# Kernel optimization log

Hardware: AMD Instinct MI355X
Metric: run time of the kernel (lower is better)

The kernel has to match this reference:

```python
import jax, jax.numpy as jnp
import numpy as np

EPS = 1e-5

def layer_norm(x, gamma, beta):
    m = jnp.mean(x, axis=-1, keepdims=True)
    v = jnp.var(x, axis=-1, keepdims=True)
    return (x - m) * jax.lax.rsqrt(v + EPS) * gamma + beta


def setup_inputs() -> dict:
    key = jax.random.key(0)
    ks = jax.random.split(key, 8)
    B, N, E, C = 1, 512, 128, 128
    s = 0.02
    inp = {
        "pair_rep": jax.random.normal(ks[0], (B, N, N, E), dtype=jnp.float32),
        "ln_pair_g": jnp.ones((E,), jnp.float32),
        "ln_pair_b": jnp.zeros((E,), jnp.float32),
        "ga_w": jax.random.normal(ks[1], (E, C), jnp.float32) * s,
        "ga_b": jnp.zeros((C,), jnp.float32),
        "la_w": jax.random.normal(ks[2], (E, C), jnp.float32) * s,
        "la_b": jnp.zeros((C,), jnp.float32),
        "gb_w": jax.random.normal(ks[3], (E, C), jnp.float32) * s,
        "gb_b": jnp.zeros((C,), jnp.float32),
        "lb_w": jax.random.normal(ks[4], (E, C), jnp.float32) * s,
        "lb_b": jnp.zeros((C,), jnp.float32),
        "g_w": jax.random.normal(ks[5], (E, E), jnp.float32) * s,
        "g_b": jnp.zeros((E,), jnp.float32),
        "ln_up_g": jnp.ones((C,), jnp.float32),
        "ln_up_b": jnp.zeros((C,), jnp.float32),
        "lu_w": jax.random.normal(ks[6], (C, E), jnp.float32) * s,
        "lu_b": jnp.zeros((E,), jnp.float32),
    }
    return inp


def reference(pair_rep, ln_pair_g, ln_pair_b, ga_w, ga_b, la_w, la_b,
              gb_w, gb_b, lb_w, lb_b, g_w, g_b, ln_up_g, ln_up_b, lu_w, lu_b):
    # pair_rep: [B, N, N, E]
    z = layer_norm(pair_rep, ln_pair_g, ln_pair_b)
    a = jax.nn.sigmoid(z @ ga_w + ga_b) * (z @ la_w + la_b)  # [B,N,N,C]
    b = jax.nn.sigmoid(z @ gb_w + gb_b) * (z @ lb_w + lb_b)  # [B,N,N,C]
    g = jax.nn.sigmoid(z @ g_w + g_b)                        # [B,N,N,E]
    # torch: sum(a.unsqueeze(-3)*b.unsqueeze(-4), dim=-2) == sum_k a[i,k,c]*b[j,k,c]
    update = jnp.einsum("bikc,bjkc->bijc", a, b)             # [B,N,N,C]
    out = g * (layer_norm(update, ln_up_g, ln_up_b) @ lu_w + lu_b)
    return out
```

## Files before the change

kernel.cpp:

```cpp
#include <hip/hip_runtime.h>
#include <hip/hip_bf16.h>

#define NN 512
#define MM (NN*NN)

typedef __attribute__((ext_vector_type(8))) unsigned short u16x8;
typedef __attribute__((ext_vector_type(4))) unsigned short u16x4;
typedef __attribute__((ext_vector_type(8))) __bf16 bf16x8;
typedef __attribute__((ext_vector_type(4))) float f32x4;

static __device__ __forceinline__ unsigned short f2bfi(float f) {
  return __builtin_bit_cast(unsigned short, __float2bfloat16(f));
}
static __device__ __forceinline__ float bf2f(unsigned short h) {
  return __uint_as_float(((unsigned int)h) << 16);
}
static __device__ __forceinline__ bf16x8 ldfrag(const unsigned short* p) {
  u16x8 v = *(const u16x8*)p;
  return __builtin_bit_cast(bf16x8, v);
}
static __device__ __forceinline__ float sigm(float x) {
  return 1.0f / (1.0f + __expf(-x));
}

__global__ void prep_weights(const float* __restrict__ ga_w, const float* __restrict__ la_w,
                             const float* __restrict__ gb_w, const float* __restrict__ lb_w,
                             const float* __restrict__ g_w,  const float* __restrict__ lu_w,
                             unsigned short* __restrict__ WT) {
  int idx = blockIdx.x * 256 + threadIdx.x;
  if (idx >= 768 * 128) return;
  int n = idx >> 7;
  int k = idx & 127;
  int grp = n >> 7, cn = n & 127;
  const float* tabs[6] = {ga_w, la_w, gb_w, lb_w, g_w, lu_w};
  WT[idx] = f2bfi(tabs[grp][k * 128 + cn]);
}

__global__ __launch_bounds__(512, 4) void k1_proj(
    const float* __restrict__ pair, const float* __restrict__ lng, const float* __restrict__ lnb,
    const unsigned short* __restrict__ WT,
    const float* __restrict__ ga_b, const float* __restrict__ la_b,
    const float* __restrict__ gb_b, const float* __restrict__ lb_b,
    const float* __restrict__ g_b,
    unsigned short* __restrict__ a_t, unsigned short* __restrict__ b_t,
    unsigned short* __restrict__ g_buf) {
  __shared__ __align__(16) unsigned short W0[128 * 136];
  __shared__ __align__(16) unsigned short W1[128 * 136];
  const int t = threadIdx.x;
  const size_t m0 = (size_t)blockIdx.x * 128;
  const int wave = t >> 6, lane = t & 63, lrow = lane & 15, qk = lane >> 4;
  const int rbase = t >> 4, off_ = (t & 15) * 8;

  u16x8 rga[4], rla[4], rgb[4], rlb[4], rg[4];
  auto stage_ld = [&](u16x8* r, int base) {
#pragma unroll
    for (int it = 0; it < 4; ++it)
      r[it] = *(const u16x8*)(WT + (size_t)(base + it * 32 + rbase) * 128 + off_);
  };
  auto stage_st = [&](unsigned short* buf, const u16x8* r) {
#pragma unroll
    for (int it = 0; it < 4; ++it)
      *(u16x8*)(buf + (it * 32 + rbase) * 136 + off_) = r[it];
  };

  stage_ld(rga, 0);
  stage_ld(rla, 128);

  {
    const int row = t >> 2, q = t & 3;
    const float* pr = pair + (m0 + row) * 128 + q * 32;
    float vals[32];
    float s = 0.f, ss = 0.f;
#pragma unroll
    for (int it = 0; it < 8; ++it) {
      f32x4 v = *(const f32x4*)(pr + it * 4);
#pragma unroll
      for (int j = 0; j < 4; ++j) { float x = v[j]; vals[it * 4 + j] = x; s += x; ss += x * x; }
    }
    s += __shfl_xor(s, 1);  s += __shfl_xor(s, 2);
    ss += __shfl_xor(ss, 1); ss += __shfl_xor(ss, 2);
    const float mean = s * (1.f / 128.f);
    const float var  = ss * (1.f / 128.f) - mean * mean;
    const float rstd = rsqrtf(var + 1e-5f);
#pragma unroll
    for (int i = 0; i < 4; ++i) {
      u16x8 pk;
#pragma unroll
      for (int j = 0; j < 8; ++j) {
        int c = q * 32 + i * 8 + j;
        pk[j] = f2bfi((vals[i * 8 + j] - mean) * rstd * lng[c] + lnb[c]);
      }
      *(u16x8*)(W0 + row * 136 + q * 32 + i * 8) = pk;
    }
  }
  __syncthreads();

  bf16x8 af[4];
  f32x4 accg[8], accl[8];
  auto run_gemm = [&](const unsigned short* buf, f32x4* acc) {
#pragma unroll
    for (int nt = 0; nt < 8; ++nt)
#pragma unroll
      for (int r = 0; r < 4; ++r) acc[nt][r] = 0.f;
#pragma unroll
    for (int ks = 0; ks < 4; ++ks)
#pragma unroll
      for (int nt = 0; nt < 8; ++nt) {
        bf16x8 bv = ldfrag(buf + (nt * 16 + lrow) * 136 + ks * 32 + 8 * qk);
        acc[nt] = __builtin_amdgcn_mfma_f32_16x16x32_bf16(af[ks], bv, acc[nt], 0, 0, 0);
      }
  };
  auto epi_ab = [&](unsigned short* buf, const float* gbias, const float* lbias) {
#pragma unroll
    for (int nt = 0; nt < 8; ++nt) {
      int col = nt * 16 + lrow;
      float bg = gbias[col], bl = lbias[col];
      u16x4 pk;
#pragma unroll
      for (int r = 0; r < 4; ++r)
        pk[r] = f2bfi(sigm(accg[nt][r] + bg) * (accl[nt][r] + bl));
      *(u16x4*)(buf + col * 136 + wave * 16 + qk * 4) = pk;
    }
  };
  auto wout = [&](unsigned short* dst, const unsigned short* buf) {
#pragma unroll
    for (int it = 0; it < 4; ++it) {
      int idx = it * 512 + t;
      int col = idx >> 4, i = idx & 15;
      *(u16x8*)(dst + (size_t)col * MM + m0 + i * 8) = *(const u16x8*)(buf + col * 136 + i * 8);
    }
  };

#pragma unroll
  for (int ks = 0; ks < 4; ++ks)
    af[ks] = ldfrag(W0 + (wave * 16 + lrow) * 136 + ks * 32 + 8 * qk);
  stage_st(W1, rga);
  stage_ld(rgb, 256);
  __syncthreads();
  run_gemm(W1, accg);
  stage_st(W0, rla);
  stage_ld(rlb, 384);
  __syncthreads();
  run_gemm(W0, accl);
  stage_st(W1, rgb);
  stage_ld(rg, 512);
  __syncthreads();
  epi_ab(W0, ga_b, la_b);
  __syncthreads();
  wout(a_t, W0);
  run_gemm(W1, accg);
  __syncthreads();
  stage_st(W0, rlb);
  stage_st(W1, rg);
  __syncthreads();
  run_gemm(W0, accl);
  __syncthreads();
  epi_ab(W0, gb_b, lb_b);
  run_gemm(W1, accg);
  __syncthreads();
  wout(b_t, W0);
#pragma unroll
  for (int nt = 0; nt < 8; ++nt) {
    int col = nt * 16 + lrow;
    float bg = g_b[col];
#pragma unroll
    for (int r = 0; r < 4; ++r)
      g_buf[(m0 + wave * 16 + qk * 4 + r) * 128 + col] = f2bfi(sigm(accg[nt][r] + bg));
  }
}

__global__ __launch_bounds__(256) void k2_einsum(
    const unsigned short* __restrict__ a_t, const unsigned short* __restrict__ b_t,
    unsigned short* __restrict__ up_t) {
  __shared__ __align__(16) unsigned short sA[2][128 * 40];
  __shared__ __align__(16) unsigned short sB[2][128 * 40];
  const int t = threadIdx.x;
  const int wid = (blockIdx.x & 7) * 256 + (blockIdx.x >> 3);
  const int c = wid >> 4;
  const int i0 = ((wid >> 2) & 3) * 128, j0 = (wid & 3) * 128;
  const unsigned short* Ag = a_t + (size_t)c * MM + (size_t)i0 * 512;
  const unsigned short* Bg = b_t + (size_t)c * MM + (size_t)j0 * 512;
  const int wave = t >> 6, lane = t & 63, wr = wave >> 1, wc = wave & 1;
  const int lrow = lane & 15, qk = lane >> 4;
  const int srow = t >> 2, sq = t & 3;
  f32x4 acc[4][4];
#pragma unroll
  for (int i = 0; i < 4; ++i)
#pragma unroll
    for (int j = 0; j < 4; ++j)
#pragma unroll
      for (int r = 0; r < 4; ++r) acc[i][j][r] = 0.f;

  u16x8 ra[2], rb[2];
  auto tile_ld = [&](int k0) {
#pragma unroll
    for (int h = 0; h < 2; ++h) {
      int row = h * 64 + srow;
      ra[h] = *(const u16x8*)(Ag + (size_t)row * 512 + k0 + sq * 8);
      rb[h] = *(const u16x8*)(Bg + (size_t)row * 512 + k0 + sq * 8);
    }
  };
  auto tile_st = [&](int buf) {
#pragma unroll
    for (int h = 0; h < 2; ++h) {
      int row = h * 64 + srow;
      *(u16x8*)(sA[buf] + row * 40 + sq * 8) = ra[h];
      *(u16x8*)(sB[buf] + row * 40 + sq * 8) = rb[h];
    }
  };

  tile_ld(0);
  tile_st(0);
  __syncthreads();
  int cur = 0;
  for (int ks = 0; ks < 16; ++ks) {
    if (ks < 15) tile_ld((ks + 1) * 32);
    bf16x8 afr[4], bv[4];
#pragma unroll
    for (int mt = 0; mt < 4; ++mt)
      afr[mt] = ldfrag(sA[cur] + (wr * 64 + mt * 16 + lrow) * 40 + 8 * qk);
#pragma unroll
    for (int nt = 0; nt < 4; ++nt)
      bv[nt] = ldfrag(sB[cur] + (wc * 64 + nt * 16 + lrow) * 40 + 8 * qk);
#pragma unroll
    for (int mt = 0; mt < 4; ++mt)
#pragma unroll
      for (int nt = 0; nt < 4; ++nt)
        acc[mt][nt] = __builtin_amdgcn_mfma_f32_16x16x32_bf16(afr[mt], bv[nt], acc[mt][nt], 0, 0, 0);
    if (ks < 15) tile_st(cur ^ 1);
    __syncthreads();
    cur ^= 1;
  }
  unsigned short* up = up_t + (size_t)c * MM;
#pragma unroll
  for (int mt = 0; mt < 4; ++mt)
#pragma unroll
    for (int nt = 0; nt < 4; ++nt) {
      int col = j0 + wc * 64 + nt * 16 + lrow;
#pragma unroll
      for (int r = 0; r < 4; ++r) {
        int row = i0 + wr * 64 + mt * 16 + qk * 4 + r;
        up[(size_t)row * 512 + col] = f2bfi(acc[mt][nt][r]);
      }
    }
}

__global__ __launch_bounds__(256) void k3_final(
    const unsigned short* __restrict__ up_t, const unsigned short* __restrict__ g_buf,
    const unsigned short* __restrict__ WT,
    const float* __restrict__ lnug, const float* __restrict__ lnub,
    const float* __restrict__ lu_b, float* __restrict__ out) {
  __shared__ __align__(16) unsigned short sU[64 * 138];
  __shared__ __align__(16) unsigned short sA[64 * 136];
  __shared__ __align__(16) unsigned short sB[128 * 136];
  const int t = threadIdx.x;
  const size_t m0 = (size_t)blockIdx.x * 64;
#pragma unroll
  for (int it = 0; it < 4; ++it) {
    int idx = it * 256 + t;
    int c = idx >> 3, m8 = (idx & 7) * 8;
    u16x8 v = *(const u16x8*)(up_t + (size_t)c * MM + m0 + m8);
#pragma unroll
    for (int j = 0; j < 8; ++j) sU[(m8 + j) * 138 + c] = v[j];
  }
#pragma unroll
  for (int it = 0; it < 8; ++it) {
    int idx = it * 256 + t;
    int n = idx >> 4, off = (idx & 15) * 8;
    *(u16x8*)(sB + n * 136 + off) = *(const u16x8*)(WT + (size_t)(640 + n) * 128 + off);
  }
  __syncthreads();
  {
    const int row = t >> 2, q = t & 3;
    float vals[32]; float s = 0.f, ss = 0.f;
#pragma unroll
    for (int jj = 0; jj < 32; ++jj) {
      int cc = q + jj * 4;
      float x = bf2f(sU[row * 138 + cc]);
      vals[jj] = x; s += x; ss += x * x;
    }
    s += __shfl_xor(s, 1);  s += __shfl_xor(s, 2);
    ss += __shfl_xor(ss, 1); ss += __shfl_xor(ss, 2);
    float mean = s * (1.f / 128.f);
    float var  = ss * (1.f / 128.f) - mean * mean;
    float rstd = rsqrtf(var + 1e-5f);
#pragma unroll
    for (int jj = 0; jj < 32; ++jj) {
      int cc = q + jj * 4;
      float zn = (vals[jj] - mean) * rstd * lnug[cc] + lnub[cc];
      sA[row * 136 + cc] = f2bfi(zn);
    }
  }
  __syncthreads();
  const int wave = t >> 6, lane = t & 63, lrow = lane & 15, qk = lane >> 4;
  f32x4 acc[8];
#pragma unroll
  for (int i = 0; i < 8; ++i)
#pragma unroll
    for (int r = 0; r < 4; ++r) acc[i][r] = 0.f;
#pragma unroll
  for (int ks = 0; ks < 4; ++ks) {
    int k0 = ks * 32;
    bf16x8 af = ldfrag(sA + (wave * 16 + lrow) * 136 + k0 + 8 * qk);
#pragma unroll
    for (int nt = 0; nt < 8; ++nt) {
      bf16x8 bv = ldfrag(sB + (nt * 16 + lrow) * 136 + k0 + 8 * qk);
      acc[nt] = __builtin_amdgcn_mfma_f32_16x16x32_bf16(af, bv, acc[nt], 0, 0, 0);
    }
  }
#pragma unroll
  for (int nt = 0; nt < 8; ++nt) {
    int e = nt * 16 + lrow;
    float bb = lu_b[e];
#pragma unroll
    for (int r = 0; r < 4; ++r) {
      size_t m = m0 + wave * 16 + qk * 4 + r;
      float lin = acc[nt][r] + bb;
      float gv = bf2f(g_buf[m * 128 + e]);
      out[m * 128 + e] = gv * lin;
    }
  }
}

extern "C" void kernel_launch(void* const* d_in, const int* in_sizes, int n_in,
                              void* d_out, int out_size, void* d_ws, size_t ws_size,
                              hipStream_t stream) {
  const float* pair = (const float*)d_in[0];
  const float* lng  = (const float*)d_in[1];
  const float* lnb  = (const float*)d_in[2];
  const float* ga_w = (const float*)d_in[3];
  const float* ga_b = (const float*)d_in[4];
  const float* la_w = (const float*)d_in[5];
  const float* la_b = (const float*)d_in[6];
  const float* gb_w = (const float*)d_in[7];
  const float* gb_b = (const float*)d_in[8];
  const float* lb_w = (const float*)d_in[9];
  const float* lb_b = (const float*)d_in[10];
  const float* g_w  = (const float*)d_in[11];
  const float* g_b  = (const float*)d_in[12];
  const float* lnug = (const float*)d_in[13];
  const float* lnub = (const float*)d_in[14];
  const float* lu_w = (const float*)d_in[15];
  const float* lu_b = (const float*)d_in[16];
  float* out = (float*)d_out;

  char* ws = (char*)d_ws;
  unsigned short* WT    = (unsigned short*)(ws);
  unsigned short* a_t   = (unsigned short*)(ws + 196608ull);
  unsigned short* b_t   = (unsigned short*)(ws + 67305472ull);
  unsigned short* g_buf = (unsigned short*)(ws + 134414336ull);
  unsigned short* up_t  = (unsigned short*)(ws + 201523200ull);

  hipLaunchKernelGGL(prep_weights, dim3(384), dim3(256), 0, stream,
                     ga_w, la_w, gb_w, lb_w, g_w, lu_w, WT);
  hipLaunchKernelGGL(k1_proj, dim3(2048), dim3(512), 0, stream,
                     pair, lng, lnb, WT, ga_b, la_b, gb_b, lb_b, g_b, a_t, b_t, g_buf);
  hipLaunchKernelGGL(k2_einsum, dim3(2048), dim3(256), 0, stream, a_t, b_t, up_t);
  hipLaunchKernelGGL(k3_final, dim3(4096), dim3(256), 0, stream,
                     up_t, g_buf, WT, lnug, lnub, lu_b, out);
}
```

Baseline: 297.7 us.

## Pre-swizzle projection weights into MFMA fragment order and read them from global

Weights for the five input projections are written by prep_weights in per-wave MFMA B-fragment order, so k1_proj loads them straight from global/L2 into registers instead of staging them through shared memory with many barriers. Each wave now owns 16 output columns across all 128 rows, and the gate and linear GEMMs are fused into one pass that shares the A fragments. The a/b epilogue goes through a small per-wave shared transpose buffer, and g is staged through shared memory so its global stores are coalesced. This removes most block-wide syncs and the weight-staging LDS traffic. In exchange, every block re-reads the weights from cache and each wave reads all the Z rows from LDS.

New measurement: 491.7 us. 1.65x slower.

```diff
diff --git a/kernel.cpp b/kernel.cpp
--- a/kernel.cpp
+++ b/kernel.cpp
@@ -26,45 +26,39 @@
 __global__ void prep_weights(const float* __restrict__ ga_w, const float* __restrict__ la_w,
                              const float* __restrict__ gb_w, const float* __restrict__ lb_w,
                              const float* __restrict__ g_w,  const float* __restrict__ lu_w,
-                             unsigned short* __restrict__ WT) {
+                             unsigned short* __restrict__ WT_lu, unsigned short* __restrict__ WF) {
   int idx = blockIdx.x * 256 + threadIdx.x;
-  if (idx >= 768 * 128) return;
-  int n = idx >> 7;
-  int k = idx & 127;
-  int grp = n >> 7, cn = n & 127;
-  const float* tabs[6] = {ga_w, la_w, gb_w, lb_w, g_w, lu_w};
-  WT[idx] = f2bfi(tabs[grp][k * 128 + cn]);
+  if (idx < 16384) {
+    int n = idx >> 7, k = idx & 127;
+    WT_lu[idx] = f2bfi(lu_w[k * 128 + n]);
+  } else {
+    int id2 = idx - 16384;
+    int j = id2 & 7, lane = (id2 >> 3) & 63, ks = (id2 >> 9) & 3, w = (id2 >> 11) & 7, gm = id2 >> 14;
+    int col = w * 16 + (lane & 15);
+    int k = ks * 32 + (lane >> 4) * 8 + j;
+    const float* tabs[5] = {ga_w, la_w, gb_w, lb_w, g_w};
+    WF[id2] = f2bfi(tabs[gm][k * 128 + col]);
+  }
 }
 
 __global__ __launch_bounds__(512, 4) void k1_proj(
     const float* __restrict__ pair, const float* __restrict__ lng, const float* __restrict__ lnb,
-    const unsigned short* __restrict__ WT,
+    const unsigned short* __restrict__ WF,
     const float* __restrict__ ga_b, const float* __restrict__ la_b,
     const float* __restrict__ gb_b, const float* __restrict__ lb_b,
     const float* __restrict__ g_b,
     unsigned short* __restrict__ a_t, unsigned short* __restrict__ b_t,
     unsigned short* __restrict__ g_buf) {
-  __shared__ __align__(16) unsigned short W0[128 * 136];
-  __shared__ __align__(16) unsigned short W1[128 * 136];
+  __shared__ __align__(16) unsigned short sZ[128 * 136];
+  __shared__ __align__(16) unsigned short sS[8 * 1088];
   const int t = threadIdx.x;
   const size_t m0 = (size_t)blockIdx.x * 128;
   const int wave = t >> 6, lane = t & 63, lrow = lane & 15, qk = lane >> 4;
-  const int rbase = t >> 4, off_ = (t & 15) * 8;
-
-  u16x8 rga[4], rla[4], rgb[4], rlb[4], rg[4];
-  auto stage_ld = [&](u16x8* r, int base) {
-#pragma unroll
-    for (int it = 0; it < 4; ++it)
-      r[it] = *(const u16x8*)(WT + (size_t)(base + it * 32 + rbase) * 128 + off_);
-  };
-  auto stage_st = [&](unsigned short* buf, const u16x8* r) {
-#pragma unroll
-    for (int it = 0; it < 4; ++it)
-      *(u16x8*)(buf + (it * 32 + rbase) * 136 + off_) = r[it];
-  };
-
-  stage_ld(rga, 0);
-  stage_ld(rla, 128);
+  const int w16 = wave * 16;
+  const int mycol = w16 + lrow;
+  const float bga = ga_b[mycol], bla = la_b[mycol];
+  const float bgb = gb_b[mycol], blb = lb_b[mycol];
+  const float bgg = g_b[mycol];
 
   {
     const int row = t >> 2, q = t & 3;
@@ -90,82 +84,88 @@
         int c = q * 32 + i * 8 + j;
         pk[j] = f2bfi((vals[i * 8 + j] - mean) * rstd * lng[c] + lnb[c]);
       }
-      *(u16x8*)(W0 + row * 136 + q * 32 + i * 8) = pk;
-    }
-  }
-  __syncthreads();
-
-  bf16x8 af[4];
+      *(u16x8*)(sZ + row * 136 + q * 32 + i * 8) = pk;
+    }
+  }
+  __syncthreads();
+
+  const unsigned short* zb = sZ + lrow * 136 + qk * 8;
+  const unsigned short* wfbase = WF + wave * 2048 + lane * 8;
   f32x4 accg[8], accl[8];
-  auto run_gemm = [&](const unsigned short* buf, f32x4* acc) {
-#pragma unroll
-    for (int nt = 0; nt < 8; ++nt)
-#pragma unroll
-      for (int r = 0; r < 4; ++r) acc[nt][r] = 0.f;
-#pragma unroll
-    for (int ks = 0; ks < 4; ++ks)
-#pragma unroll
-      for (int nt = 0; nt < 8; ++nt) {
-        bf16x8 bv = ldfrag(buf + (nt * 16 + lrow) * 136 + ks * 32 + 8 * qk);
-        acc[nt] = __builtin_amdgcn_mfma_f32_16x16x32_bf16(af[ks], bv, acc[nt], 0, 0, 0);
-      }
+
+  auto pair_pass = [&](const unsigned short* wf1, const unsigned short* wf2) {
+#pragma unroll
+    for (int m = 0; m < 8; ++m)
+#pragma unroll
+      for (int r = 0; r < 4; ++r) { accg[m][r] = 0.f; accl[m][r] = 0.f; }
+#pragma unroll
+    for (int ks = 0; ks < 4; ++ks) {
+      bf16x8 b1 = ldfrag(wf1 + ks * 512);
+      bf16x8 b2 = ldfrag(wf2 + ks * 512);
+#pragma unroll
+      for (int m = 0; m < 8; ++m) {
+        bf16x8 av = ldfrag(zb + m * 2176 + ks * 32);
+        accg[m] = __builtin_amdgcn_mfma_f32_16x16x32_bf16(av, b1, accg[m], 0, 0, 0);
+        accl[m] = __builtin_amdgcn_mfma_f32_16x16x32_bf16(av, b2, accl[m], 0, 0, 0);
+      }
+    }
   };
-  auto epi_ab = [&](unsigned short* buf, const float* gbias, const float* lbias) {
-#pragma unroll
-    for (int nt = 0; nt < 8; ++nt) {
-      int col = nt * 16 + lrow;
-      float bg = gbias[col], bl = lbias[col];
-      u16x4 pk;
-#pragma unroll
-      for (int r = 0; r < 4; ++r)
-        pk[r] = f2bfi(sigm(accg[nt][r] + bg) * (accl[nt][r] + bl));
-      *(u16x4*)(buf + col * 136 + wave * 16 + qk * 4) = pk;
+
+  auto epi_ab = [&](unsigned short* dst, float bg, float bl) {
+    unsigned short* st = sS + wave * 1088;
+#pragma unroll
+    for (int half = 0; half < 2; ++half) {
+#pragma unroll
+      for (int mm = 0; mm < 4; ++mm) {
+        int m = half * 4 + mm;
+        u16x4 pk;
+#pragma unroll
+        for (int r = 0; r < 4; ++r)
+          pk[r] = f2bfi(sigm(accg[m][r] + bg) * (accl[m][r] + bl));
+        *(u16x4*)(st + lrow * 68 + mm * 16 + qk * 4) = pk;
+      }
+      int c4 = lane >> 2, rq = lane & 3;
+      u16x8 v0 = *(const u16x8*)(st + c4 * 68 + rq * 16);
+      u16x8 v1 = *(const u16x8*)(st + c4 * 68 + rq * 16 + 8);
+      unsigned short* dp = dst + (size_t)(w16 + c4) * MM + m0 + half * 64 + rq * 16;
+      *(u16x8*)dp = v0;
+      *(u16x8*)(dp + 8) = v1;
     }
   };
-  auto wout = [&](unsigned short* dst, const unsigned short* buf) {
-#pragma unroll
-    for (int it = 0; it < 4; ++it) {
-      int idx = it * 512 + t;
-      int col = idx >> 4, i = idx & 15;
-      *(u16x8*)(dst + (size_t)col * MM + m0 + i * 8) = *(const u16x8*)(buf + col * 136 + i * 8);
-    }
-  };
-
-#pragma unroll
-  for (int ks = 0; ks < 4; ++ks)
-    af[ks] = ldfrag(W0 + (wave * 16 + lrow) * 136 + ks * 32 + 8 * qk);
-  stage_st(W1, rga);
-  stage_ld(rgb, 256);
-  __syncthreads();
-  run_gemm(W1, accg);
-  stage_st(W0, rla);
-  stage_ld(rlb, 384);
-  __syncthreads();
-  run_gemm(W0, accl);
-  stage_st(W1, rgb);
-  stage_ld(rg, 512);
-  __syncthreads();
-  epi_ab(W0, ga_b, la_b);
-  __syncthreads();
-  wout(a_t, W0);
-  run_gemm(W1, accg);
-  __syncthreads();
-  stage_st(W0, rlb);
-  stage_st(W1, rg);
-  __syncthreads();
-  run_gemm(W0, accl);
-  __syncthreads();
-  epi_ab(W0, gb_b, lb_b);
-  run_gemm(W1, accg);
-  __syncthreads();
-  wout(b_t, W0);
-#pragma unroll
-  for (int nt = 0; nt < 8; ++nt) {
-    int col = nt * 16 + lrow;
-    float bg = g_b[col];
+
+  pair_pass(wfbase, wfbase + 16384);
+  epi_ab(a_t, bga, bla);
+  pair_pass(wfbase + 2 * 16384, wfbase + 3 * 16384);
+  epi_ab(b_t, bgb, blb);
+
+  {
+    const unsigned short* wf = wfbase + 4 * 16384;
+#pragma unroll
+    for (int m = 0; m < 8; ++m)
+#pragma unroll
+      for (int r = 0; r < 4; ++r) accg[m][r] = 0.f;
+#pragma unroll
+    for (int ks = 0; ks < 4; ++ks) {
+      bf16x8 b1 = ldfrag(wf + ks * 512);
+#pragma unroll
+      for (int m = 0; m < 8; ++m) {
+        bf16x8 av = ldfrag(zb + m * 2176 + ks * 32);
+        accg[m] = __builtin_amdgcn_mfma_f32_16x16x32_bf16(av, b1, accg[m], 0, 0, 0);
+      }
+    }
+  }
+  __syncthreads();
+#pragma unroll
+  for (int m = 0; m < 8; ++m)
 #pragma unroll
     for (int r = 0; r < 4; ++r)
-      g_buf[(m0 + wave * 16 + qk * 4 + r) * 128 + col] = f2bfi(sigm(accg[nt][r] + bg));
+      sZ[(m * 16 + qk * 4 + r) * 136 + mycol] = f2bfi(sigm(accg[m][r] + bgg));
+  __syncthreads();
+#pragma unroll
+  for (int it = 0; it < 4; ++it) {
+    int idx = it * 512 + t;
+    int mr = idx >> 4, off = (idx & 15) * 8;
+    *(u16x8*)(g_buf + (m0 + mr) * 128 + off) = *(const u16x8*)(sZ + mr * 136 + off);
   }
 }
 
@@ -247,7 +247,7 @@
 
 __global__ __launch_bounds__(256) void k3_final(
     const unsigned short* __restrict__ up_t, const unsigned short* __restrict__ g_buf,
-    const unsigned short* __restrict__ WT,
+    const unsigned short* __restrict__ WT_lu,
     const float* __restrict__ lnug, const float* __restrict__ lnub,
     const float* __restrict__ lu_b, float* __restrict__ out) {
   __shared__ __align__(16) unsigned short sU[64 * 138];
@@ -267,7 +267,7 @@
   for (int it = 0; it < 8; ++it) {
     int idx = it * 256 + t;
     int n = idx >> 4, off = (idx & 15) * 8;
-    *(u16x8*)(sB + n * 136 + off) = *(const u16x8*)(WT + (size_t)(640 + n) * 128 + off);
+    *(u16x8*)(sB + n * 136 + off) = *(const u16x8*)(WT_lu + (size_t)n * 128 + off);
   }
   __syncthreads();
   {
@@ -345,17 +345,18 @@
   float* out = (float*)d_out;
 
   char* ws = (char*)d_ws;
-  unsigned short* WT    = (unsigned short*)(ws);
-  unsigned short* a_t   = (unsigned short*)(ws + 196608ull);
-  unsigned short* b_t   = (unsigned short*)(ws + 67305472ull);
-  unsigned short* g_buf = (unsigned short*)(ws + 134414336ull);
-  unsigned short* up_t  = (unsigned short*)(ws + 201523200ull);
+  unsigned short* WT_lu = (unsigned short*)(ws);
+  unsigned short* WF    = (unsigned short*)(ws + 32768ull);
+  unsigned short* a_t   = (unsigned short*)(ws + 360448ull);
+  unsigned short* b_t   = (unsigned short*)(ws + 67469312ull);
+  unsigned short* g_buf = (unsigned short*)(ws + 134578176ull);
+  unsigned short* up_t  = (unsigned short*)(ws + 201687040ull);
 
   hipLaunchKernelGGL(prep_weights, dim3(384), dim3(256), 0, stream,
-                     ga_w, la_w, gb_w, lb_w, g_w, lu_w, WT);
+                     ga_w, la_w, gb_w, lb_w, g_w, lu_w, WT_lu, WF);
   hipLaunchKernelGGL(k1_proj, dim3(2048), dim3(512), 0, stream,
-                     pair, lng, lnb, WT, ga_b, la_b, gb_b, lb_b, g_b, a_t, b_t, g_buf);
+                     pair, lng, lnb, WF, ga_b, la_b, gb_b, lb_b, g_b, a_t, b_t, g_buf);
   hipLaunchKernelGGL(k2_einsum, dim3(2048), dim3(256), 0, stream, a_t, b_t, up_t);
   hipLaunchKernelGGL(k3_final, dim3(4096), dim3(256), 0, stream,
-                     up_t, g_buf, WT, lnug, lnub, lu_b, out);
-}
+                     up_t, g_buf, WT_lu, lnug, lnub, lu_b, out);
+}
```
